# Optimization experiments

Hardware: AMD Instinct MI355X
Metric: run time of the kernel (lower is better)

Reference implementation:

```python
import jax, jax.numpy as jnp
import numpy as np

L = 8192   # sequence length
B = 4      # batch
D = 512    # embed_dim
NDIM = 16  # EMA state dim
Z = 128    # shared q/k dim
W = 128    # attention window
MP = 256   # max relative positions
NEG = -50000.0  # TOKEN_SELF_ATTN_VALUE-style mask fill


def setup_inputs() -> dict:
    key = jax.random.key(0)
    ks = jax.random.split(key, 16)
    def tn(k, shp, std):  # truncated-normal-ish init (clipped normal)
        return jnp.clip(jax.random.normal(k, shp) * std, -2 * std, 2 * std)
    val = jnp.ones((NDIM, 1)).at[1::2].set(-1.0)  # MultiHeadEMA beta init pattern
    return {
        "x": jax.random.normal(ks[0], (L, B, D), dtype=jnp.float32),
        "delta": tn(ks[1], (D, NDIM, 1), 0.2),
        "alpha": tn(ks[2], (D, NDIM, 1), 0.2),
        "beta": tn(ks[3], (D, NDIM, 1), 0.02) + val,
        "gamma": jax.random.normal(ks[4], (D, NDIM)),
        "omega": jax.random.normal(ks[5], (D,)),
        "Wp": tn(ks[6], (D, 1), 0.02),      # LatentConfigurator weight_proj
        "bp": jnp.zeros((1,)),
        "temp": jnp.array([0.5 * np.log(D)], dtype=jnp.float32),  # log(sqrt(D))
        "Wz": tn(ks[7], (D, Z), 0.02),
        "qg": jax.random.normal(ks[8], (Z,)) * 0.02 + 1.0,
        "qb": jnp.zeros((Z,)),
        "kg": jax.random.normal(ks[9], (Z,)) * 0.02 + 1.0,
        "kb": jnp.zeros((Z,)),
        "Wv": tn(ks[10], (D, D), 0.02),
        "relb": tn(ks[11], (2 * MP - 1,), 0.02),  # FastRelativePositionalBias table
    }


def _rotary(t, cos, sin):
    # t: (B, L, Z); cos/sin: (L, Z//2). Complex rotation on interleaved pairs.
    t1, t2 = t[..., 0::2], t[..., 1::2]
    return jnp.stack([t1 * cos - t2 * sin, t1 * sin + t2 * cos], axis=-1).reshape(t.shape)


def _forward(x, delta, alpha, beta, gamma, omega, Wp, bp, temp, Wz, qg, qb, kg, kb, Wv, relb):
    scale = 1.0 / np.sqrt(NDIM)
    # ---- MultiHeadEMA: damped EMA as long convolution via FFT ----
    p = jax.nn.sigmoid(delta)                      # (D,N,1)
    a = jax.nn.sigmoid(alpha)
    logq = jnp.log1p(-(p * a))                     # log(1 - p*alpha)
    t = jnp.arange(L, dtype=jnp.float32)
    kern = (p * beta) * jnp.exp(logq * t)          # (D,N,L) Vandermonde kernel
    k1d = jnp.einsum('dnl,dn->dl', kern, gamma * scale)  # (D,L)
    xb = x.transpose(1, 2, 0)                      # (B,D,L)
    conv = jnp.fft.irfft(jnp.fft.rfft(xb, n=2 * L) * jnp.fft.rfft(k1d, n=2 * L), n=2 * L)[..., :L]
    mx = jax.nn.silu(conv.transpose(2, 0, 1) + x * omega)  # (L,B,D)
    # ---- LatentConfigurator: sigmoid token routing (proj_dim==1) ----
    pi = jax.nn.sigmoid((mx @ Wp + bp) / jnp.exp(temp))[..., 0].T  # (B,L)
    mxb = mx.transpose(1, 0, 2)                    # (B,L,D)
    sel = pi > 0.5
    idx = jnp.cumsum(sel.astype(jnp.int32), axis=1) * sel  # (B,L); 0 -> dropped slot
    counts = sel.sum(axis=1)                       # (B,)
    bi = jnp.arange(B)[:, None]
    # compress_seq: scatter selected tokens to compact prefix (slot 0 dropped)
    c = jnp.zeros((B, L + 1, D), mx.dtype).at[bi, idx].add(mxb * sel[..., None])[:, 1:]
    # ---- windowed attention over compressed tokens ----
    z = jax.nn.silu(c @ Wz)                        # (B,L,Z)
    freqs = 1.0 / (10000.0 ** (jnp.arange(0, Z, 2, dtype=jnp.float32) / Z))
    ang = jnp.arange(L, dtype=jnp.float32)[:, None] * freqs
    cos, sin = jnp.cos(ang), jnp.sin(ang)
    q = _rotary(z * qg + qb, cos, sin)
    kk = _rotary(z * kg + kb, cos, sin)
    v = jax.nn.silu(c @ Wv)                        # (B,L,D)
    n = L // W
    qw = q.reshape(B, n, W, Z)
    def look_around(tw):  # prepend previous window: (B,n,W,f) -> (B,n,2W,f)
        prev = jnp.pad(tw, ((0, 0), (1, 0), (0, 0), (0, 0)))[:, :-1]
        return jnp.concatenate([prev, tw], axis=2)
    kw = look_around(kk.reshape(B, n, W, Z))
    vw = look_around(v.reshape(B, n, W, D))
    base = (jnp.arange(n) * W)[:, None, None]
    qabs = base + jnp.arange(W)[None, :, None]         # (n,W,1)
    kabs = base + jnp.arange(-W, W)[None, None, :]     # (n,1,2W)
    mask = (kabs <= qabs) & (kabs >= 0) & (kabs[None] < counts[:, None, None, None])  # (B,n,W,2W)
    rel = jnp.arange(-W, W)[None, :] - jnp.arange(W)[:, None]   # (W,2W)
    bias = relb[jnp.clip(rel + MP - 1, 0, 2 * MP - 2)]          # (W,2W)
    scores = jnp.einsum('bnwz,bnkz->bnwk', qw, kw) / np.sqrt(Z) + bias
    attn = jax.nn.softmax(jnp.where(mask, scores, NEG), axis=-1)
    h = jnp.einsum('bnwk,bnkd->bnwd', attn, vw).reshape(B, L, D)
    # ---- extract: gather back to original positions, gate by pi ----
    hpad = jnp.concatenate([jnp.zeros((B, 1, D), h.dtype), h], axis=1)
    hsel = jnp.take_along_axis(hpad, idx[..., None], axis=1)    # (B,L,D)
    return x + (hsel * pi[..., None]).transpose(1, 0, 2)        # (L,B,D)


def reference(x, delta, alpha, beta, gamma, omega, Wp, bp, temp, Wz, qg, qb, kg, kb, Wv, relb):
    return _forward(x, delta, alpha, beta, gamma, omega, Wp, bp, temp, Wz, qg, qb, kg, kb, Wv, relb)
```

## Files before the change

### kernel.cpp

```cpp
#include <hip/hip_runtime.h>
#include <math.h>

constexpr int L = 8192;
constexpr int B = 4;
constexpr int D = 512;
constexpr int NDIM = 16;
constexpr int Z = 128;
constexpr float NEGF = -50000.0f;
constexpr int CCL = 64;
constexpr int NCH = L / CCL;
constexpr int FMAX = 64;

typedef short s16x8 __attribute__((ext_vector_type(8)));
typedef float f32x4 __attribute__((ext_vector_type(4)));

typedef __attribute__((address_space(1))) const void* as1cv;
typedef __attribute__((address_space(3))) void* as3v;

__device__ __forceinline__ void gld16(const void* g, void* l) {
  __builtin_amdgcn_global_load_lds((as1cv)g, (as3v)l, 16, 0, 0);
}

__device__ __forceinline__ unsigned short f2bf(float f) {
  unsigned u = __builtin_bit_cast(unsigned, f);
  u += 0x7fffu + ((u >> 16) & 1u);
  return (unsigned short)(u >> 16);
}

#define DPPADD(acc, ctrl, rmask)                                                   \
  {                                                                                \
    int _mv = __builtin_amdgcn_update_dpp(0, __builtin_bit_cast(int, acc),         \
                                          ctrl, rmask, 0xf, false);                \
    acc += __builtin_bit_cast(float, _mv);                                         \
  }

__global__ __launch_bounds__(256) void k_prep(const float* __restrict__ delta,
                                              const float* __restrict__ alpha,
                                              const float* __restrict__ beta,
                                              const float* __restrict__ gamma,
                                              double* __restrict__ qdn,
                                              double* __restrict__ cdn,
                                              double* __restrict__ rp1,
                                              double* __restrict__ rp2,
                                              float* __restrict__ qf,
                                              float* __restrict__ cf,
                                              float* __restrict__ r1f,
                                              float* __restrict__ r2f,
                                              int* __restrict__ fcnt) {
  int i = blockIdx.x * 256 + threadIdx.x;
  if (i == 0) *fcnt = 0;
  if (i >= D * NDIM) return;
  double p = 1.0 / (1.0 + exp(-(double)delta[i]));
  double a = 1.0 / (1.0 + exp(-(double)alpha[i]));
  double q = 1.0 - p * a;
  double c = p * (double)beta[i] * (double)gamma[i] * 0.25;
  qdn[i] = q; cdn[i] = c;
  double q2 = q * q, q4 = q2 * q2, q8 = q4 * q4;
  double q16 = q8 * q8, q32 = q16 * q16, q64 = q32 * q32;
  rp1[i] = q64;
  rp2[i] = q64 * q64;
  qf[i] = (float)q; cf[i] = (float)c;
  r1f[i] = (float)q64; r2f[i] = (float)(q64 * q64);
}

__global__ __launch_bounds__(256) void k_tab(float2* __restrict__ tab) {
  int tid = blockIdx.x * 256 + threadIdx.x;
  int i = tid & 63, j = tid >> 6;
  double freq = exp(((double)(-2 * i) / 128.0) * log(10000.0));
  float angf = (float)j * (float)freq;
  double sa, ca;
  sincos((double)angf, &sa, &ca);
  float2 r; r.x = (float)ca; r.y = (float)sa;
  tab[tid] = r;
}

__global__ __launch_bounds__(256) void k_convA(const float* __restrict__ x,
                                               const float* __restrict__ qf,
                                               float* __restrict__ E) {
  int bx = blockIdx.x;
  int tile = bx & 31, dg = (bx >> 5) & 7, b = bx >> 8;
  int dl = threadIdx.x & 63, cl = threadIdx.x >> 6;
  int dgl = dg * 64 + dl;
  int t = tile * 4 + cl;
  float q[NDIM], s[NDIM];
#pragma unroll
  for (int n = 0; n < NDIM; ++n) { q[n] = qf[dgl * NDIM + n]; s[n] = 0.f; }
  const float* xp = x + ((size_t)(t * CCL) * B + b) * D + dgl;
#pragma unroll
  for (int ii = 0; ii < CCL; ii += 32) {
    float xv[32];
#pragma unroll
    for (int u = 0; u < 32; ++u) xv[u] = xp[(ii + u) * (B * D)];
#pragma unroll
    for (int u = 0; u < 32; ++u) {
#pragma unroll
      for (int n = 0; n < NDIM; ++n) s[n] = fmaf(q[n], s[n], xv[u]);
    }
  }
  float* eb = E + ((size_t)(b * NCH + t) * NDIM) * 512 + dgl;
#pragma unroll
  for (int n = 0; n < NDIM; ++n) eb[(size_t)n * 512] = s[n];
}

__global__ __launch_bounds__(256) void k_convC(const float* __restrict__ x,
                                               const float* __restrict__ omega,
                                               const float* __restrict__ qf,
                                               const float* __restrict__ cf,
                                               const float* __restrict__ r1f,
                                               const float* __restrict__ r2f,
                                               const float* __restrict__ E,
                                               const float* __restrict__ Wp,
                                               unsigned short* __restrict__ mxb,
                                               float* __restrict__ pdot) {
  int bx = blockIdx.x;
  int tile = bx & 31, dg = (bx >> 5) & 7, b = bx >> 8;
  int dl = threadIdx.x & 63, cl = threadIdx.x >> 6;
  int dgl = dg * 64 + dl;
  int t = tile * 4 + cl;
  float q[NDIM], c[NDIM], s[NDIM];
#pragma unroll
  for (int n = 0; n < NDIM; ++n) {
    q[n] = qf[dgl * NDIM + n];
    c[n] = cf[dgl * NDIM + n];
    s[n] = 0.f;
  }
  if (t >= 1) {
    const float* e1 = E + ((size_t)(b * NCH + t - 1) * NDIM) * 512 + dgl;
#pragma unroll
    for (int n = 0; n < NDIM; ++n) s[n] = e1[(size_t)n * 512];
  }
  if (t >= 2) {
    const float* e2 = E + ((size_t)(b * NCH + t - 2) * NDIM) * 512 + dgl;
#pragma unroll
    for (int n = 0; n < NDIM; ++n) s[n] = fmaf(r1f[dgl * NDIM + n], e2[(size_t)n * 512], s[n]);
  }
  if (t >= 3) {
    const float* e3 = E + ((size_t)(b * NCH + t - 3) * NDIM) * 512 + dgl;
#pragma unroll
    for (int n = 0; n < NDIM; ++n) s[n] = fmaf(r2f[dgl * NDIM + n], e3[(size_t)n * 512], s[n]);
  }
  float om = omega[dgl];
  float wp = Wp[dgl];
  const float* xp = x + ((size_t)(t * CCL) * B + b) * D + dgl;
  unsigned short* mp = mxb + ((size_t)b * L + t * CCL) * 512 + dgl;
  float* pp = pdot + ((size_t)(b * L + t * CCL)) * 8 + dg;
#pragma unroll
  for (int ii = 0; ii < CCL; ii += 32) {
    float xv[32];
#pragma unroll
    for (int u = 0; u < 32; ++u) xv[u] = xp[(ii + u) * (B * D)];
#pragma unroll
    for (int u = 0; u < 32; ++u) {
      int i = ii + u;
#pragma unroll
      for (int n = 0; n < NDIM; ++n) s[n] = fmaf(q[n], s[n], xv[u]);
      float p0 = c[0] * s[0], p1 = c[1] * s[1], p2 = c[2] * s[2], p3 = c[3] * s[3];
      p0 = fmaf(c[4], s[4], p0);  p1 = fmaf(c[5], s[5], p1);
      p2 = fmaf(c[6], s[6], p2);  p3 = fmaf(c[7], s[7], p3);
      p0 = fmaf(c[8], s[8], p0);  p1 = fmaf(c[9], s[9], p1);
      p2 = fmaf(c[10], s[10], p2); p3 = fmaf(c[11], s[11], p3);
      p0 = fmaf(c[12], s[12], p0); p1 = fmaf(c[13], s[13], p1);
      p2 = fmaf(c[14], s[14], p2); p3 = fmaf(c[15], s[15], p3);
      float conv = (p0 + p1) + (p2 + p3);
      float m = fmaf(xv[u], om, conv);
      float v = m / (1.0f + __expf(-m));
      mp[(size_t)i * 512] = f2bf(v);
      float pd = v * wp;
      DPPADD(pd, 0x111, 0xf);
      DPPADD(pd, 0x112, 0xf);
      DPPADD(pd, 0x114, 0xf);
      DPPADD(pd, 0x118, 0xf);
      DPPADD(pd, 0x142, 0xa);
      DPPADD(pd, 0x143, 0x8);
      if (dl == 63) pp[(size_t)i * 8] = pd;
    }
  }
}

__global__ __launch_bounds__(256) void k_logitc(const float* __restrict__ pdot,
                                                const float* __restrict__ bp,
                                                const float* __restrict__ temp,
                                                float* __restrict__ pi,
                                                int* __restrict__ selb,
                                                int* __restrict__ fcnt,
                                                int* __restrict__ flags) {
  int rid = blockIdx.x * 256 + threadIdx.x;
  const float* pr = pdot + (size_t)rid * 8;
  double acc = 0.0;
#pragma unroll
  for (int j = 0; j < 8; ++j) acc += (double)pr[j];
  double logit = acc + (double)bp[0];
  pi[rid] = (float)(1.0 / (1.0 + exp(-logit / exp((double)temp[0]))));
  selb[rid] = (logit > 0.0) ? 1 : 0;
  if (fabs(logit) < 1e-4) {
    int slot = atomicAdd(fcnt, 1);
    if (slot < FMAX) flags[slot] = rid;
  }
}

__global__ __launch_bounds__(256) void k_fix(const int* __restrict__ fcnt,
                                             const int* __restrict__ flags,
                                             const float* __restrict__ x,
                                             const double* __restrict__ qdn,
                                             const double* __restrict__ cdn,
                                             const double* __restrict__ rp1,
                                             const double* __restrict__ rp2,
                                             const float* __restrict__ omega,
                                             const float* __restrict__ Wp,
                                             double* __restrict__ pfix) {
  int nb = blockIdx.x;
  int fi = nb >> 3, dblk = nb & 7;
  int count = *fcnt; if (count > FMAX) count = FMAX;
  if (fi >= count) return;
  int rid = flags[fi];
  int b = rid >> 13, l = rid & (L - 1);
  int t = l >> 6, io = l & 63;
  int sub = threadIdx.x >> 6, dl = threadIdx.x & 63;
  int d = dblk * 64 + dl;
  double q[NDIM], s[NDIM];
#pragma unroll
  for (int n = 0; n < NDIM; ++n) { q[n] = qdn[d * NDIM + n]; s[n] = 0.0; }
  int c0 = (sub < 3) ? (t - 3 + sub) : t;
  int steps = (sub < 3) ? 64 : (io + 1);
  if (c0 >= 0) {
    const float* xp = x + ((size_t)(c0 * CCL) * B + b) * D + d;
    for (int i = 0; i < steps; ++i) {
      double xv = (double)xp[(size_t)i * (B * D)];
#pragma unroll
      for (int n = 0; n < NDIM; ++n) s[n] = fma(q[n], s[n], xv);
    }
  }
  __shared__ double Esm[4][64][NDIM];
#pragma unroll
  for (int n = 0; n < NDIM; ++n) Esm[sub][dl][n] = s[n];
  __syncthreads();
  if (sub == 3) {
    double sfin[NDIM];
#pragma unroll
    for (int n = 0; n < NDIM; ++n) {
      double base = q[n], r = 1.0;
      int e = io + 1;
      while (e) { if (e & 1) r *= base; base *= base; e >>= 1; }
      double S = Esm[2][dl][n] + rp1[d * NDIM + n] * Esm[1][dl][n] + rp2[d * NDIM + n] * Esm[0][dl][n];
      sfin[n] = Esm[3][dl][n] + r * S;
    }
    double conv = 0.0;
#pragma unroll
    for (int n = 0; n < NDIM; ++n) conv = fma(cdn[d * NDIM + n], sfin[n], conv);
    double xv = (double)x[((size_t)l * B + b) * D + d];
    double m = conv + xv * (double)omega[d];
    double mxd = m / (1.0 + exp(-m));
    double v = mxd * (double)Wp[d];
#pragma unroll
    for (int off = 32; off; off >>= 1) v += __shfl_down(v, off, 64);
    if (dl == 0) pfix[fi * 8 + dblk] = v;
  }
}

__global__ __launch_bounds__(64) void k_fix2(const int* __restrict__ fcnt,
                                             const int* __restrict__ flags,
                                             const double* __restrict__ pfix,
                                             const float* __restrict__ bp,
                                             const float* __restrict__ temp,
                                             float* __restrict__ pi,
                                             int* __restrict__ selb) {
  int fi = threadIdx.x;
  int count = *fcnt; if (count > FMAX) count = FMAX;
  if (fi >= count) return;
  double s = 0.0;
#pragma unroll
  for (int j = 0; j < 8; ++j) s += pfix[fi * 8 + j];
  double logit = s + (double)bp[0];
  int rid = flags[fi];
  selb[rid] = (logit > 0.0) ? 1 : 0;
  pi[rid] = (float)(1.0 / (1.0 + exp(-logit / exp((double)temp[0]))));
}

__global__ __launch_bounds__(256) void k_scan(const int* __restrict__ selb,
                                              int* __restrict__ idx,
                                              int* __restrict__ src,
                                              int* __restrict__ counts) {
  int b = blockIdx.x;
  int t = threadIdx.x;
  __shared__ int part[256];
  const int PER = L / 256;
  int base = b * L + t * PER;
  int loc[PER];
  int cnt = 0;
#pragma unroll
  for (int i = 0; i < PER; ++i) { loc[i] = selb[base + i]; cnt += loc[i]; }
  part[t] = cnt;
  __syncthreads();
  for (int off = 1; off < 256; off <<= 1) {
    int v = (t >= off) ? part[t - off] : 0;
    __syncthreads();
    part[t] += v;
    __syncthreads();
  }
  int run = (t == 0) ? 0 : part[t - 1];
#pragma unroll
  for (int i = 0; i < PER; ++i) {
    int sflag = loc[i];
    run += sflag;
    idx[base + i] = sflag ? run : 0;
    if (sflag) src[b * L + run - 1] = t * PER + i;
  }
  if (t == 255) counts[b] = part[255];
  __syncthreads();
  int total = part[255];
  for (int i2 = total + t; i2 < L; i2 += 256) src[b * L + i2] = 0;
}

__global__ __launch_bounds__(256) void k_wt(const float* __restrict__ Wm,
                                            unsigned short* __restrict__ Wt, int N) {
  int idx = blockIdx.x * 256 + threadIdx.x;
  int n = idx >> 9, kk = idx & 511;
  Wt[idx] = f2bf(Wm[(size_t)kk * N + n]);
}

__global__ __launch_bounds__(256) void k_gemm_mfma(const unsigned short* __restrict__ mxb,
                                                   const int* __restrict__ src,
                                                   const int* __restrict__ counts,
                                                   const unsigned short* __restrict__ Bt,
                                                   float* __restrict__ outF,
                                                   unsigned short* __restrict__ outT,
                                                   int N, int mode) {
  __shared__ char smem[32768];
  char* As = smem;
  char* Bs = smem + 16384;
  int tid = threadIdx.x;
  int w = tid >> 6, l = tid & 63;
  int mtile, ntile;
  if (mode == 1) {
    int lin = blockIdx.y * 256 + blockIdx.x;
    int xcd = lin & 7, loc = lin >> 3;
    mtile = xcd * 32 + (loc >> 2);
    ntile = loc & 3;
  } else {
    mtile = blockIdx.x; ntile = blockIdx.y;
  }
  int m0 = mtile * 128, n0 = ntile * 128;
  int gb = m0 >> 13, j0 = m0 & 8191;
  if (j0 >= counts[gb]) return;
  int wr = w >> 1, wc = w & 1;
  const unsigned short* arow[4];
  const unsigned short* brow[4];
#pragma unroll
  for (int ld = 0; ld < 4; ++ld) {
    int li = w * 4 + ld;
    int row = li * 8 + (l >> 3);
    int col = ((l & 7) ^ (row & 7)) << 3;
    int srow = src[gb * 8192 + j0 + row];
    arow[ld] = mxb + ((size_t)gb * 8192 + srow) * 512 + col;
    brow[ld] = Bt + (size_t)(n0 + row) * 512 + col;
  }
  f32x4 acc[4][4];
  f32x4 zz = {0.f, 0.f, 0.f, 0.f};
#pragma unroll
  for (int mi = 0; mi < 4; ++mi)
#pragma unroll
    for (int ni = 0; ni < 4; ++ni) acc[mi][ni] = zz;

  for (int k0 = 0; k0 < 512; k0 += 64) {
#pragma unroll
    for (int ld = 0; ld < 4; ++ld) {
      int li = w * 4 + ld;
      gld16(arow[ld] + k0, As + li * 1024);
      gld16(brow[ld] + k0, Bs + li * 1024);
    }
    __syncthreads();
    s16x8 af[4][2], bfr[4][2];
#pragma unroll
    for (int kh = 0; kh < 2; ++kh) {
#pragma unroll
      for (int mi = 0; mi < 4; ++mi) {
        int row = wr * 64 + mi * 16 + (l & 15);
        int byte = row * 128 + ((kh * 64 + ((l >> 4) * 16)) ^ ((row & 7) << 4));
        af[mi][kh] = *(const s16x8*)(As + byte);
      }
#pragma unroll
      for (int ni = 0; ni < 4; ++ni) {
        int row = wc * 64 + ni * 16 + (l & 15);
        int byte = row * 128 + ((kh * 64 + ((l >> 4) * 16)) ^ ((row & 7) << 4));
        bfr[ni][kh] = *(const s16x8*)(Bs + byte);
      }
    }
#pragma unroll
    for (int kh = 0; kh < 2; ++kh)
#pragma unroll
      for (int mi = 0; mi < 4; ++mi)
#pragma unroll
        for (int ni = 0; ni < 4; ++ni)
          acc[mi][ni] = __builtin_amdgcn_mfma_f32_16x16x32_bf16(af[mi][kh], bfr[ni][kh], acc[mi][ni], 0, 0, 0);
    __syncthreads();
  }
  if (mode == 0) {
#pragma unroll
    for (int mi = 0; mi < 4; ++mi)
#pragma unroll
      for (int ni = 0; ni < 4; ++ni)
#pragma unroll
        for (int r = 0; r < 4; ++r) {
          float vv = acc[mi][ni][r];
          vv = vv / (1.0f + __expf(-vv));
          int mrow = m0 + wr * 64 + mi * 16 + (l >> 4) * 4 + r;
          int ncol = n0 + wc * 64 + ni * 16 + (l & 15);
          outF[(size_t)mrow * N + ncol] = vv;
        }
  } else {
#pragma unroll
    for (int mi = 0; mi < 4; ++mi)
#pragma unroll
      for (int ni = 0; ni < 4; ++ni)
#pragma unroll
        for (int r = 0; r < 4; ++r) {
          float vv = acc[mi][ni][r];
          vv = vv / (1.0f + __expf(-vv));
          int mrow = wr * 64 + mi * 16 + (l >> 4) * 4 + r;
          int ncol = wc * 64 + ni * 16 + (l & 15);
          int byteoff = ncol * 256 + ((mrow * 2) ^ ((ncol & 7) << 4));
          *(unsigned short*)(smem + byteoff) = f2bf(vv);
        }
    __syncthreads();
#pragma unroll
    for (int it = 0; it < 8; ++it) {
      int ncol = w * 32 + it * 4 + (l >> 4);
      int ch = l & 15;
      int byteoff = ncol * 256 + ((ch * 16) ^ ((ncol & 7) << 4));
      s16x8 vch = *(const s16x8*)(smem + byteoff);
      *(s16x8*)(outT + ((size_t)(gb * 512 + n0 + ncol)) * 8192 + j0 + ch * 8) = vch;
    }
  }
}

__global__ __launch_bounds__(256) void k_rot(const float* __restrict__ z,
                                             const float2* __restrict__ tab,
                                             const int* __restrict__ counts,
                                             const float* __restrict__ qg,
                                             const float* __restrict__ qb,
                                             const float* __restrict__ kg,
                                             const float* __restrict__ kb,
                                             unsigned short* __restrict__ qo,
                                             unsigned short* __restrict__ ko) {
  int tid = blockIdx.x * 256 + threadIdx.x;
  int i = tid & 63;
  int row = tid >> 6;
  int j = row & (L - 1);
  int b = row >> 13;
  if (j >= counts[b]) return;
  float2 cs = tab[j * 64 + i];
  float cc = cs.x, ss = cs.y;
  size_t base = (size_t)row * Z + 2 * i;
  float z1 = z[base], z2 = z[base + 1];
  float q1 = z1 * qg[2 * i] + qb[2 * i], q2 = z2 * qg[2 * i + 1] + qb[2 * i + 1];
  float k1 = z1 * kg[2 * i] + kb[2 * i], k2 = z2 * kg[2 * i + 1] + kb[2 * i + 1];
  qo[base]     = f2bf(q1 * cc - q2 * ss);
  qo[base + 1] = f2bf(q1 * ss + q2 * cc);
  ko[base]     = f2bf(k1 * cc - k2 * ss);
  ko[base + 1] = f2bf(k1 * ss + k2 * cc);
}

__global__ __launch_bounds__(256) void k_attn_mfma(const unsigned short* __restrict__ q,
                                                   const unsigned short* __restrict__ k,
                                                   const unsigned short* __restrict__ vT,
                                                   const float* __restrict__ relb,
                                                   const int* __restrict__ counts,
                                                   const int* __restrict__ src,
                                                   const float* __restrict__ pi,
                                                   const float* __restrict__ x,
                                                   float* __restrict__ out) {
  __shared__ char smem[81920];
  char* Qs = smem;
  char* Ks = smem + 16384;
  char* Ps = smem;
  char* Vs = smem + 32768;
  int tid = threadIdx.x, w = tid >> 6, l = tid & 63;
  int bid = blockIdx.x;
  int n = bid & 63, b = (bid >> 6) & 3, half = bid >> 8;
  int cnt = counts[b];
  int q0 = n * 128 + half * 64;
  if (q0 >= cnt) return;
  int kbase = n * 128 - 128;
  const size_t rowb = (size_t)b * L;

#pragma unroll
  for (int ld = 0; ld < 4; ++ld) {
    int li = w * 4 + ld;
    int row = li * 4 + (l >> 4);
    int colb = ((l & 15) * 16) ^ ((row & 7) << 4);
    gld16((const char*)(q + (rowb + q0 + row) * Z) + colb, Qs + li * 1024);
  }
#pragma unroll
  for (int ld = 0; ld < 16; ++ld) {
    int li = w * 16 + ld;
    int row = li * 4 + (l >> 4);
    int jk = kbase + row; if (jk < 0) jk = 0;
    int colb = ((l & 15) * 16) ^ ((row & 7) << 4);
    gld16((const char*)(k + (rowb + jk) * Z) + colb, Ks + li * 1024);
  }
  __syncthreads();

  int m0 = w * 16;
  f32x4 s[16];
  f32x4 zz = {0.f, 0.f, 0.f, 0.f};
#pragma unroll
  for (int ni = 0; ni < 16; ++ni) s[ni] = zz;
  s16x8 aq[4];
#pragma unroll
  for (int ks = 0; ks < 4; ++ks) {
    int row = m0 + (l & 15);
    int byte = row * 256 + ((ks * 64 + ((l >> 4) * 16)) ^ ((row & 7) << 4));
    aq[ks] = *(const s16x8*)(Qs + byte);
  }
#pragma unroll
  for (int ni = 0; ni < 16; ++ni) {
    int row = ni * 16 + (l & 15);
    int rb = row * 256, sw = (row & 7) << 4;
#pragma unroll
    for (int ks = 0; ks < 4; ++ks) {
      s16x8 bk = *(const s16x8*)(Ks + rb + ((ks * 64 + ((l >> 4) * 16)) ^ sw));
      s[ni] = __builtin_amdgcn_mfma_f32_16x16x32_bf16(aq[ks], bk, s[ni], 0, 0, 0);
    }
  }
  __syncthreads();

  auto stageV = [&](int nc) {
#pragma unroll
    for (int ld = 0; ld < 8; ++ld) {
      int li = w * 8 + ld;
      int row = li * 2 + (l >> 5);
      int colb = ((l & 31) * 16) ^ ((row & 7) << 4);
      int j = kbase + (colb >> 1);
      if (j < 0) j = 0;
      gld16((const char*)(vT + ((size_t)(b * 512 + nc * 64 + row)) * L + j), Vs + li * 1024);
    }
  };
  stageV(0);

  int rgrp = (l >> 4) * 4;
  float mxr[4] = {-3e38f, -3e38f, -3e38f, -3e38f};
#pragma unroll
  for (int ni = 0; ni < 16; ++ni) {
    int col = ni * 16 + (l & 15);
    int kabs = kbase + col;
#pragma unroll
    for (int r = 0; r < 4; ++r) {
      int ww = half * 64 + m0 + rgrp + r;
      bool valid = (kabs >= 0) && (kabs <= n * 128 + ww) && (kabs < cnt);
      float vv = valid ? (s[ni][r] * 0.08838834764831845f + relb[col + 127 - ww]) : NEGF;
      s[ni][r] = vv;
      mxr[r] = fmaxf(mxr[r], vv);
    }
  }
#pragma unroll
  for (int r = 0; r < 4; ++r)
    for (int off = 1; off < 16; off <<= 1)
      mxr[r] = fmaxf(mxr[r], __shfl_xor(mxr[r], off, 64));
  float smr[4] = {0.f, 0.f, 0.f, 0.f};
#pragma unroll
  for (int ni = 0; ni < 16; ++ni)
#pragma unroll
    for (int r = 0; r < 4; ++r) {
      float p = __expf(s[ni][r] - mxr[r]);
      s[ni][r] = p;
      smr[r] += p;
    }
#pragma unroll
  for (int r = 0; r < 4; ++r) {
    for (int off = 1; off < 16; off <<= 1) smr[r] += __shfl_xor(smr[r], off, 64);
    smr[r] = 1.0f / smr[r];
  }
#pragma unroll
  for (int ni = 0; ni < 16; ++ni) {
    int colb2 = (ni * 16 + (l & 15)) * 2;
#pragma unroll
    for (int r = 0; r < 4; ++r) {
      int row = m0 + rgrp + r;
      *(unsigned short*)(Ps + row * 512 + (colb2 ^ ((row & 7) << 4))) = f2bf(s[ni][r] * smr[r]);
    }
  }
  __syncthreads();

  int tlr[4]; float pvr[4]; bool vr[4];
#pragma unroll
  for (int r = 0; r < 4; ++r) {
    int jq = q0 + m0 + rgrp + r;
    vr[r] = (jq < cnt);
    int tl = vr[r] ? src[(b << 13) + jq] : 0;
    tlr[r] = tl;
    pvr[r] = pi[(b << 13) + tl];
  }

  for (int nc = 0; nc < 8; ++nc) {
    if (nc) {
      __syncthreads();
      stageV(nc);
      __syncthreads();
    }
    f32x4 o[4];
#pragma unroll
    for (int ni = 0; ni < 4; ++ni) o[ni] = zz;
    int prow = m0 + (l & 15);
    int psw = (prow & 7) << 4;
#pragma unroll
    for (int kt = 0; kt < 4; ++kt) {
      s16x8 pa0 = *(const s16x8*)(Ps + prow * 512 + ((kt * 128 + ((l >> 4) * 16)) ^ psw));
      s16x8 pa1 = *(const s16x8*)(Ps + prow * 512 + ((kt * 128 + 64 + ((l >> 4) * 16)) ^ psw));
#pragma unroll
      for (int ni = 0; ni < 4; ++ni) {
        int vrow = ni * 16 + (l & 15);
        int vsw = (vrow & 7) << 4;
        s16x8 vb0 = *(const s16x8*)(Vs + vrow * 512 + ((kt * 128 + ((l >> 4) * 16)) ^ vsw));
        s16x8 vb1 = *(const s16x8*)(Vs + vrow * 512 + ((kt * 128 + 64 + ((l >> 4) * 16)) ^ vsw));
        o[ni] = __builtin_amdgcn_mfma_f32_16x16x32_bf16(pa0, vb0, o[ni], 0, 0, 0);
        o[ni] = __builtin_amdgcn_mfma_f32_16x16x32_bf16(pa1, vb1, o[ni], 0, 0, 0);
      }
    }
#pragma unroll
    for (int ni = 0; ni < 4; ++ni)
#pragma unroll
      for (int r = 0; r < 4; ++r)
        if (vr[r]) {
          size_t off = ((size_t)tlr[r] * B + b) * 512 + nc * 64 + ni * 16 + (l & 15);
          out[off] = fmaf(o[ni][r], pvr[r], x[off]);
        }
  }
}

__global__ __launch_bounds__(256) void k_fill(const float* __restrict__ x,
                                              const int* __restrict__ idx,
                                              float* __restrict__ out) {
  int e4 = blockIdx.x * 256 + threadIdx.x;
  int rem = e4 >> 7;
  int b = rem & 3;
  int l = rem >> 2;
  if (idx[(b << 13) + l] == 0)
    ((float4*)out)[e4] = ((const float4*)x)[e4];
}

extern "C" void kernel_launch(void* const* d_in, const int* in_sizes, int n_in,
                              void* d_out, int out_size, void* d_ws, size_t ws_size,
                              hipStream_t stream) {
  const float* x     = (const float*)d_in[0];
  const float* delta = (const float*)d_in[1];
  const float* alpha = (const float*)d_in[2];
  const float* beta  = (const float*)d_in[3];
  const float* gamma = (const float*)d_in[4];
  const float* omega = (const float*)d_in[5];
  const float* Wp    = (const float*)d_in[6];
  const float* bp    = (const float*)d_in[7];
  const float* temp  = (const float*)d_in[8];
  const float* Wz    = (const float*)d_in[9];
  const float* qg    = (const float*)d_in[10];
  const float* qb    = (const float*)d_in[11];
  const float* kg    = (const float*)d_in[12];
  const float* kb    = (const float*)d_in[13];
  const float* Wv    = (const float*)d_in[14];
  const float* relb  = (const float*)d_in[15];
  (void)in_sizes; (void)n_in; (void)out_size; (void)ws_size;

  char* wsb = (char*)d_ws;
  size_t o = 0;
  auto alloc = [&](size_t bytes) {
    char* p = wsb + o;
    o += (bytes + 255) & ~(size_t)255;
    return p;
  };
  unsigned short* mxb  = (unsigned short*)alloc((size_t)B * L * D * 4);
  float* Ebuf          = (float*)((char*)mxb + (size_t)B * L * D * 2);
  float* zb            = (float*)alloc((size_t)B * L * Z * 4);
  unsigned short* qb2  = (unsigned short*)alloc((size_t)B * L * Z * 2);
  unsigned short* kb2  = (unsigned short*)alloc((size_t)B * L * Z * 2);
  unsigned short* vTb  = (unsigned short*)alloc((size_t)B * D * L * 2);
  unsigned short* wzt  = (unsigned short*)alloc((size_t)Z * 512 * 2);
  unsigned short* wvt  = (unsigned short*)alloc((size_t)D * 512 * 2);
  float2* tab = (float2*)alloc((size_t)L * 64 * 8);
  float* pdot = (float*)alloc((size_t)B * L * 8 * 4);
  float* pib  = (float*)alloc((size_t)B * L * 4);
  int* selb   = (int*)alloc((size_t)B * L * 4);
  int* idx    = (int*)alloc((size_t)B * L * 4);
  int* src    = (int*)alloc((size_t)B * L * 4);
  int* cnt    = (int*)alloc(256);
  double* qdn = (double*)alloc((size_t)D * NDIM * 8);
  double* cdn = (double*)alloc((size_t)D * NDIM * 8);
  double* rp1 = (double*)alloc((size_t)D * NDIM * 8);
  double* rp2 = (double*)alloc((size_t)D * NDIM * 8);
  float* qf   = (float*)alloc((size_t)D * NDIM * 4);
  float* cf   = (float*)alloc((size_t)D * NDIM * 4);
  float* r1f  = (float*)alloc((size_t)D * NDIM * 4);
  float* r2f  = (float*)alloc((size_t)D * NDIM * 4);
  int* fcnt   = (int*)alloc(256);
  int* flags  = (int*)alloc(FMAX * 4);
  double* pfix = (double*)alloc((size_t)FMAX * 8 * 8);

  k_prep<<<(D * NDIM + 255) / 256, 256, 0, stream>>>(delta, alpha, beta, gamma,
                                                     qdn, cdn, rp1, rp2, qf, cf, r1f, r2f, fcnt);
  k_tab<<<L * 64 / 256, 256, 0, stream>>>(tab);
  k_convA<<<B * 8 * 32, 256, 0, stream>>>(x, qf, Ebuf);
  k_convC<<<B * 8 * 32, 256, 0, stream>>>(x, omega, qf, cf, r1f, r2f, Ebuf, Wp, mxb, pdot);
  k_logitc<<<B * L / 256, 256, 0, stream>>>(pdot, bp, temp, pib, selb, fcnt, flags);
  k_fix<<<FMAX * 8, 256, 0, stream>>>(fcnt, flags, x, qdn, cdn, rp1, rp2, omega, Wp, pfix);
  k_fix2<<<1, 64, 0, stream>>>(fcnt, flags, pfix, bp, temp, pib, selb);
  k_scan<<<B, 256, 0, stream>>>(selb, idx, src, cnt);
  k_wt<<<Z * 512 / 256, 256, 0, stream>>>(Wz, wzt, Z);
  k_wt<<<D * 512 / 256, 256, 0, stream>>>(Wv, wvt, D);
  k_gemm_mfma<<<dim3(256, 1), 256, 0, stream>>>(mxb, src, cnt, wzt, zb, vTb, Z, 0);
  k_gemm_mfma<<<dim3(256, 4), 256, 0, stream>>>(mxb, src, cnt, wvt, zb, vTb, D, 1);
  k_rot<<<B * L * (Z / 2) / 256, 256, 0, stream>>>(zb, tab, cnt, qg, qb, kg, kb, qb2, kb2);
  k_fill<<<(int)((size_t)L * B * D / 4 / 256), 256, 0, stream>>>(x, idx, (float*)d_out);
  k_attn_mfma<<<512, 256, 0, stream>>>(qb2, kb2, vTb, relb, cnt, src, pib, x, (float*)d_out);
}
```

Before: 225.4 us.

## Load Q, K and V operands directly from global memory in attention kernel

The attention kernel no longer stages Q, K and V tiles in shared memory through async LDS loads. Each lane reads its MFMA operands straight from global memory (relying on L2/L1 caching). The P matrix is loaded into registers once and reused across all 32 output-dimension tiles. This shrinks LDS from 80KB to 32KB and removes most barriers, which should raise occupancy. The cost is uncoalesced, repeated global reads of K and V, and higher register pressure from holding P fragments.

```diff
diff --git a/kernel.cpp b/kernel.cpp
--- a/kernel.cpp
+++ b/kernel.cpp
@@ -469,11 +469,7 @@
                                                    const float* __restrict__ pi,
                                                    const float* __restrict__ x,
                                                    float* __restrict__ out) {
-  __shared__ char smem[81920];
-  char* Qs = smem;
-  char* Ks = smem + 16384;
-  char* Ps = smem;
-  char* Vs = smem + 32768;
+  __shared__ char Ps[32768];
   int tid = threadIdx.x, w = tid >> 6, l = tid & 63;
   int bid = blockIdx.x;
   int n = bid & 63, b = (bid >> 6) & 3, half = bid >> 8;
@@ -482,62 +478,32 @@
   if (q0 >= cnt) return;
   int kbase = n * 128 - 128;
   const size_t rowb = (size_t)b * L;
-
-#pragma unroll
-  for (int ld = 0; ld < 4; ++ld) {
-    int li = w * 4 + ld;
-    int row = li * 4 + (l >> 4);
-    int colb = ((l & 15) * 16) ^ ((row & 7) << 4);
-    gld16((const char*)(q + (rowb + q0 + row) * Z) + colb, Qs + li * 1024);
-  }
-#pragma unroll
-  for (int ld = 0; ld < 16; ++ld) {
-    int li = w * 16 + ld;
-    int row = li * 4 + (l >> 4);
-    int jk = kbase + row; if (jk < 0) jk = 0;
-    int colb = ((l & 15) * 16) ^ ((row & 7) << 4);
-    gld16((const char*)(k + (rowb + jk) * Z) + colb, Ks + li * 1024);
-  }
-  __syncthreads();
-
   int m0 = w * 16;
+  int lg = l >> 4;
+
   f32x4 s[16];
   f32x4 zz = {0.f, 0.f, 0.f, 0.f};
 #pragma unroll
   for (int ni = 0; ni < 16; ++ni) s[ni] = zz;
   s16x8 aq[4];
-#pragma unroll
-  for (int ks = 0; ks < 4; ++ks) {
-    int row = m0 + (l & 15);
-    int byte = row * 256 + ((ks * 64 + ((l >> 4) * 16)) ^ ((row & 7) << 4));
-    aq[ks] = *(const s16x8*)(Qs + byte);
+  {
+    const unsigned short* qrow = q + (rowb + q0 + m0 + (l & 15)) * Z + lg * 8;
+#pragma unroll
+    for (int ks = 0; ks < 4; ++ks) aq[ks] = *(const s16x8*)(qrow + ks * 32);
   }
 #pragma unroll
   for (int ni = 0; ni < 16; ++ni) {
-    int row = ni * 16 + (l & 15);
-    int rb = row * 256, sw = (row & 7) << 4;
+    int krow = kbase + ni * 16 + (l & 15);
+    if (krow < 0) krow = 0;
+    const unsigned short* kr = k + (rowb + krow) * Z + lg * 8;
 #pragma unroll
     for (int ks = 0; ks < 4; ++ks) {
-      s16x8 bk = *(const s16x8*)(Ks + rb + ((ks * 64 + ((l >> 4) * 16)) ^ sw));
+      s16x8 bk = *(const s16x8*)(kr + ks * 32);
       s[ni] = __builtin_amdgcn_mfma_f32_16x16x32_bf16(aq[ks], bk, s[ni], 0, 0, 0);
     }
   }
-  __syncthreads();
-
-  auto stageV = [&](int nc) {
-#pragma unroll
-    for (int ld = 0; ld < 8; ++ld) {
-      int li = w * 8 + ld;
-      int row = li * 2 + (l >> 5);
-      int colb = ((l & 31) * 16) ^ ((row & 7) << 4);
-      int j = kbase + (colb >> 1);
-      if (j < 0) j = 0;
-      gld16((const char*)(vT + ((size_t)(b * 512 + nc * 64 + row)) * L + j), Vs + li * 1024);
-    }
-  };
-  stageV(0);
-
-  int rgrp = (l >> 4) * 4;
+
+  int rgrp = lg * 4;
   float mxr[4] = {-3e38f, -3e38f, -3e38f, -3e38f};
 #pragma unroll
   for (int ni = 0; ni < 16; ++ni) {
@@ -581,6 +547,15 @@
   }
   __syncthreads();
 
+  s16x8 pa[8];
+  {
+    int prow = m0 + (l & 15);
+    int psw = (prow & 7) << 4;
+#pragma unroll
+    for (int kt = 0; kt < 8; ++kt)
+      pa[kt] = *(const s16x8*)(Ps + prow * 512 + ((kt * 64 + lg * 16) ^ psw));
+  }
+
   int tlr[4]; float pvr[4]; bool vr[4];
 #pragma unroll
   for (int r = 0; r < 4; ++r) {
@@ -590,40 +565,29 @@
     tlr[r] = tl;
     pvr[r] = pi[(b << 13) + tl];
   }
-
-  for (int nc = 0; nc < 8; ++nc) {
-    if (nc) {
-      __syncthreads();
-      stageV(nc);
-      __syncthreads();
-    }
-    f32x4 o[4];
-#pragma unroll
-    for (int ni = 0; ni < 4; ++ni) o[ni] = zz;
-    int prow = m0 + (l & 15);
-    int psw = (prow & 7) << 4;
-#pragma unroll
-    for (int kt = 0; kt < 4; ++kt) {
-      s16x8 pa0 = *(const s16x8*)(Ps + prow * 512 + ((kt * 128 + ((l >> 4) * 16)) ^ psw));
-      s16x8 pa1 = *(const s16x8*)(Ps + prow * 512 + ((kt * 128 + 64 + ((l >> 4) * 16)) ^ psw));
-#pragma unroll
-      for (int ni = 0; ni < 4; ++ni) {
-        int vrow = ni * 16 + (l & 15);
-        int vsw = (vrow & 7) << 4;
-        s16x8 vb0 = *(const s16x8*)(Vs + vrow * 512 + ((kt * 128 + ((l >> 4) * 16)) ^ vsw));
-        s16x8 vb1 = *(const s16x8*)(Vs + vrow * 512 + ((kt * 128 + 64 + ((l >> 4) * 16)) ^ vsw));
-        o[ni] = __builtin_amdgcn_mfma_f32_16x16x32_bf16(pa0, vb0, o[ni], 0, 0, 0);
-        o[ni] = __builtin_amdgcn_mfma_f32_16x16x32_bf16(pa1, vb1, o[ni], 0, 0, 0);
+  int koff[8];
+#pragma unroll
+  for (int kt = 0; kt < 8; ++kt) {
+    int o2 = kbase + kt * 32 + lg * 8;
+    koff[kt] = o2 < 0 ? 0 : o2;
+  }
+
+  const unsigned short* vrow0 = vT + ((size_t)(b * 512 + (l & 15))) * L;
+#pragma unroll 2
+  for (int dt = 0; dt < 32; ++dt) {
+    const unsigned short* vr0 = vrow0 + (size_t)(dt * 16) * L;
+    f32x4 o = zz;
+#pragma unroll
+    for (int kt = 0; kt < 8; ++kt) {
+      s16x8 bv = *(const s16x8*)(vr0 + koff[kt]);
+      o = __builtin_amdgcn_mfma_f32_16x16x32_bf16(pa[kt], bv, o, 0, 0, 0);
+    }
+#pragma unroll
+    for (int r = 0; r < 4; ++r)
+      if (vr[r]) {
+        size_t off = ((size_t)tlr[r] * B + b) * 512 + dt * 16 + (l & 15);
+        out[off] = fmaf(o[r], pvr[r], x[off]);
       }
-    }
-#pragma unroll
-    for (int ni = 0; ni < 4; ++ni)
-#pragma unroll
-      for (int r = 0; r < 4; ++r)
-        if (vr[r]) {
-          size_t off = ((size_t)tlr[r] * B + b) * 512 + nc * 64 + ni * 16 + (l & 15);
-          out[off] = fmaf(o[ni][r], pvr[r], x[off]);
-        }
   }
 }
 
```

New measurement: 278.9 us. 23.7% more time.

## Double-buffer V tiles and hoist P fragments into registers in attention kernel

Applied to the files above, without the earlier changes.

The attention kernel now stages the V tile for the next 64-column chunk into a second LDS buffer while MFMAs run on the current chunk. This replaces the two barriers per chunk with one, so global-to-LDS loads overlap with compute. The P-matrix fragments are loaded from LDS once into registers instead of being re-read in every chunk. In exchange, LDS per block grows from 80KB to 96KB, which may drop the CU from two resident blocks to one, and register pressure rises.

```diff
diff --git a/kernel.cpp b/kernel.cpp
--- a/kernel.cpp
+++ b/kernel.cpp
@@ -469,11 +469,12 @@
                                                    const float* __restrict__ pi,
                                                    const float* __restrict__ x,
                                                    float* __restrict__ out) {
-  __shared__ char smem[81920];
+  __shared__ char smem[98304];
   char* Qs = smem;
   char* Ks = smem + 16384;
   char* Ps = smem;
-  char* Vs = smem + 32768;
+  char* Vb0 = smem + 32768;
+  char* Vb1 = smem + 65536;
   int tid = threadIdx.x, w = tid >> 6, l = tid & 63;
   int bid = blockIdx.x;
   int n = bid & 63, b = (bid >> 6) & 3, half = bid >> 8;
@@ -524,7 +525,7 @@
   }
   __syncthreads();
 
-  auto stageV = [&](int nc) {
+  auto stageV = [&](int nc, char* vb) {
 #pragma unroll
     for (int ld = 0; ld < 8; ++ld) {
       int li = w * 8 + ld;
@@ -532,10 +533,10 @@
       int colb = ((l & 31) * 16) ^ ((row & 7) << 4);
       int j = kbase + (colb >> 1);
       if (j < 0) j = 0;
-      gld16((const char*)(vT + ((size_t)(b * 512 + nc * 64 + row)) * L + j), Vs + li * 1024);
+      gld16((const char*)(vT + ((size_t)(b * 512 + nc * 64 + row)) * L + j), vb + li * 1024);
     }
   };
-  stageV(0);
+  stageV(0, Vb0);
 
   int rgrp = (l >> 4) * 4;
   float mxr[4] = {-3e38f, -3e38f, -3e38f, -3e38f};
@@ -581,6 +582,15 @@
   }
   __syncthreads();
 
+  s16x8 pa[8];
+  {
+    int prow = m0 + (l & 15);
+    int psw = (prow & 7) << 4;
+#pragma unroll
+    for (int kt = 0; kt < 8; ++kt)
+      pa[kt] = *(const s16x8*)(Ps + prow * 512 + ((kt * 64 + ((l >> 4) * 16)) ^ psw));
+  }
+
   int tlr[4]; float pvr[4]; bool vr[4];
 #pragma unroll
   for (int r = 0; r < 4; ++r) {
@@ -592,26 +602,22 @@
   }
 
   for (int nc = 0; nc < 8; ++nc) {
-    if (nc) {
-      __syncthreads();
-      stageV(nc);
-      __syncthreads();
-    }
+    char* vb = (nc & 1) ? Vb1 : Vb0;
+    if (nc < 7) stageV(nc + 1, (nc & 1) ? Vb0 : Vb1);
     f32x4 o[4];
 #pragma unroll
     for (int ni = 0; ni < 4; ++ni) o[ni] = zz;
-    int prow = m0 + (l & 15);
-    int psw = (prow & 7) << 4;
+    int psw2 = 0; (void)psw2;
 #pragma unroll
     for (int kt = 0; kt < 4; ++kt) {
-      s16x8 pa0 = *(const s16x8*)(Ps + prow * 512 + ((kt * 128 + ((l >> 4) * 16)) ^ psw));
-      s16x8 pa1 = *(const s16x8*)(Ps + prow * 512 + ((kt * 128 + 64 + ((l >> 4) * 16)) ^ psw));
+      s16x8 pa0 = pa[kt * 2];
+      s16x8 pa1 = pa[kt * 2 + 1];
 #pragma unroll
       for (int ni = 0; ni < 4; ++ni) {
         int vrow = ni * 16 + (l & 15);
         int vsw = (vrow & 7) << 4;
-        s16x8 vb0 = *(const s16x8*)(Vs + vrow * 512 + ((kt * 128 + ((l >> 4) * 16)) ^ vsw));
-        s16x8 vb1 = *(const s16x8*)(Vs + vrow * 512 + ((kt * 128 + 64 + ((l >> 4) * 16)) ^ vsw));
+        s16x8 vb0 = *(const s16x8*)(vb + vrow * 512 + ((kt * 128 + ((l >> 4) * 16)) ^ vsw));
+        s16x8 vb1 = *(const s16x8*)(vb + vrow * 512 + ((kt * 128 + 64 + ((l >> 4) * 16)) ^ vsw));
         o[ni] = __builtin_amdgcn_mfma_f32_16x16x32_bf16(pa0, vb0, o[ni], 0, 0, 0);
         o[ni] = __builtin_amdgcn_mfma_f32_16x16x32_bf16(pa1, vb1, o[ni], 0, 0, 0);
       }
@@ -624,6 +630,7 @@
           size_t off = ((size_t)tlr[r] * B + b) * 512 + nc * 64 + ni * 16 + (l & 15);
           out[off] = fmaf(o[ni][r], pvr[r], x[off]);
         }
+    if (nc < 7) __syncthreads();
   }
 }
 
```

Measured after the change: 260.5 us. 1.16x slower.
